# Kernel tuning notes

Hardware: AMD Instinct MI355X
Metric: run time of the kernel (lower is better)

## Reference

```python
import jax, jax.numpy as jnp
import numpy as np
import math

B, C, T = 2, 1024, 2048
H, G = 16, 32            # num_heads, groupnorm groups (channels=1024 -> 32 groups)
CH = C // H              # 64 head channels
EPS = 1e-5


def setup_inputs() -> dict:
    key = jax.random.key(0)
    ks = jax.random.split(key, 5)
    x = jax.random.normal(ks[0], (B, C, T), dtype=jnp.float32)
    # causal mask, identical across batch (matches how tortoise uses it; also makes
    # the torch mask.repeat(n_heads,1,1) tiling-order quirk a no-op)
    mask = jnp.broadcast_to(jnp.tril(jnp.ones((T, T), dtype=bool)), (B, T, T))
    qk_bias = jax.random.normal(ks[1], (1, T, T), dtype=jnp.float32) * 0.01
    gn_scale = jnp.ones((C,), dtype=jnp.float32)
    gn_bias = jnp.zeros((C,), dtype=jnp.float32)
    qkv_w = jax.random.normal(ks[2], (3 * C, C), dtype=jnp.float32) / math.sqrt(C)
    qkv_b = jnp.zeros((3 * C,), dtype=jnp.float32)
    # proj_out is zero-initialized in the module; use small random weights so the
    # attention path actually contributes (post-training regime)
    proj_w = jax.random.normal(ks[3], (C, C), dtype=jnp.float32) * 0.02
    proj_b = jnp.zeros((C,), dtype=jnp.float32)
    return {"x": x, "mask": mask, "qk_bias": qk_bias, "gn_scale": gn_scale,
            "gn_bias": gn_bias, "qkv_w": qkv_w, "qkv_b": qkv_b,
            "proj_w": proj_w, "proj_b": proj_b}


def _group_norm(x, scale, bias):
    # x: [B, C, T], normalize over (C//G, T) within each of G groups, in fp32
    xg = x.reshape(B, G, C // G, T)
    mean = xg.mean(axis=(2, 3), keepdims=True)
    var = ((xg - mean) ** 2).mean(axis=(2, 3), keepdims=True)
    xn = ((xg - mean) * jax.lax.rsqrt(var + EPS)).reshape(B, C, T)
    return xn * scale[None, :, None] + bias[None, :, None]


def reference(x, mask, qk_bias, gn_scale, gn_bias, qkv_w, qkv_b, proj_w, proj_b):
    xn = _group_norm(x, gn_scale, gn_bias)                      # [B, C, T]
    qkv = jnp.einsum('oc,bct->bot', qkv_w, xn) + qkv_b[None, :, None]  # [B, 3C, T]
    # legacy layout: width splits as (H, 3*ch)
    qkv = qkv.reshape(B * H, 3 * CH, T)
    q, k, v = qkv[:, :CH], qkv[:, CH:2 * CH], qkv[:, 2 * CH:]   # [B*H, ch, T]
    scale = 1.0 / math.sqrt(math.sqrt(CH))
    w = jnp.einsum('bct,bcs->bts', q * scale, k * scale)        # [B*H, T, T]
    w = w + qk_bias
    mask_r = jnp.tile(mask, (H, 1, 1))                          # matches torch repeat
    w = jnp.where(mask_r, w, -jnp.inf)
    w = jax.nn.softmax(w.astype(jnp.float32), axis=-1).astype(q.dtype)
    a = jnp.einsum('bts,bcs->bct', w, v).reshape(B, C, T)       # [B, C, T]
    h = jnp.einsum('oc,bct->bot', proj_w, a) + proj_b[None, :, None]
    return xn + h                                               # x_proj is Identity on normed x
```

## Files before the change

kernel.cpp:

```cpp
#include <hip/hip_runtime.h>
#include <stdint.h>

#define Tdim 2048
#define Cdim 1024
#define C3   3072

typedef __attribute__((ext_vector_type(8))) short s16x8;
typedef __attribute__((ext_vector_type(4))) unsigned short u16x4;
typedef __attribute__((ext_vector_type(2))) float f32x2;
typedef __attribute__((ext_vector_type(4))) float f32x4;
typedef __attribute__((ext_vector_type(16))) float f32x16;
typedef __attribute__((ext_vector_type(4))) int i32x4;

__device__ __forceinline__ unsigned short f2bf(float f) {
  uint32_t u = __float_as_uint(f);
  return (unsigned short)((u + 0x7FFFu + ((u >> 16) & 1u)) >> 16);
}
__device__ __forceinline__ float bf2f(unsigned short s) {
  return __uint_as_float(((uint32_t)s) << 16);
}
__device__ __forceinline__ uint32_t cvtpk(float lo, float hi) {
  uint32_t r;
  asm("v_cvt_pk_bf16_f32 %0, %1, %2" : "=v"(r) : "v"(lo), "v"(hi));
  return r;
}
__device__ __forceinline__ float exp2v(float x) {
  float r;
  asm("v_exp_f32 %0, %1" : "=v"(r) : "v"(x));
  return r;
}
typedef __attribute__((address_space(3))) unsigned char lds_uc;
typedef __attribute__((address_space(1))) const unsigned char glb_uc;
__device__ __forceinline__ void gload16(const void* g, void* l) {
  __builtin_amdgcn_global_load_lds((glb_uc*)g, (lds_uc*)l, 16, 0, 0);
}

__global__ __launch_bounds__(256) void k_prep(const float* __restrict__ x,
                                              float* __restrict__ part,
                                              const float* __restrict__ qkv_w,
                                              const float* __restrict__ proj_w,
                                              unsigned short* __restrict__ wqkv,
                                              unsigned short* __restrict__ wproj,
                                              const float* __restrict__ qk_bias,
                                              unsigned short* __restrict__ biasT) {
  __shared__ float r1[4], r2[4];
  __shared__ unsigned short L[64][65];
  int bid = blockIdx.x;
  int u = threadIdx.x;
  if (bid < 512) {
    int bg = bid >> 3, tc = bid & 7;
    const float* xp = x + ((size_t)(bg >> 5) * Cdim + (size_t)(bg & 31) * 32) * Tdim + tc * 256;
    float s1 = 0.f, s2 = 0.f;
#pragma unroll
    for (int i = 0; i < 32; ++i) {
      int e = u + i * 256;
      float v = xp[(size_t)(e >> 8) * Tdim + (e & 255)];
      s1 += v; s2 += v * v;
    }
    for (int m = 1; m < 64; m <<= 1) { s1 += __shfl_xor(s1, m); s2 += __shfl_xor(s2, m); }
    int w = u >> 6;
    if ((u & 63) == 0) { r1[w] = s1; r2[w] = s2; }
    __syncthreads();
    if (u == 0) {
      part[bid * 2]     = r1[0] + r1[1] + r1[2] + r1[3];
      part[bid * 2 + 1] = r2[0] + r2[1] + r2[2] + r2[3];
    }
  } else if (bid < 512 + 4096) {
    const int n0 = 3072 * 1024 / 4;
    int i = (bid - 512) * 256 + u;
    const float* in = qkv_w;
    unsigned short* out = wqkv;
    if (i >= n0) { i -= n0; in = proj_w; out = wproj; }
    f32x4 v = *(const f32x4*)(in + (size_t)i * 4);
    u16x4 o;
    o[0] = f2bf(v[0]); o[1] = f2bf(v[1]); o[2] = f2bf(v[2]); o[3] = f2bf(v[3]);
    *(u16x4*)(out + (size_t)i * 4) = o;
  } else {
    const float LOG2E = 1.4426950408889634f;
    int idx = bid - 4608;
    int bs0 = (idx & 31) * 64;
    int bt0 = (idx >> 5) * 64;
    int tl = u >> 2, c0 = (u & 3) * 16;
    const float* ip = qk_bias + (size_t)(bt0 + tl) * Tdim + bs0 + c0;
#pragma unroll
    for (int i = 0; i < 16; ++i) L[tl][c0 + i] = f2bf(ip[i] * LOG2E);
    __syncthreads();
    unsigned short* op = biasT + (size_t)(bs0 + tl) * Tdim + bt0 + c0;
#pragma unroll
    for (int i = 0; i < 16; i += 4) {
      u16x4 o;
      o[0] = L[c0 + i][tl]; o[1] = L[c0 + i + 1][tl];
      o[2] = L[c0 + i + 2][tl]; o[3] = L[c0 + i + 3][tl];
      *(u16x4*)(op + i) = o;
    }
  }
}

__global__ void k_gn_final(const float* __restrict__ part, float* __restrict__ stats) {
  int bg = threadIdx.x;
  float s1 = 0.f, s2 = 0.f;
  for (int j = 0; j < 8; ++j) { s1 += part[(bg * 8 + j) * 2]; s2 += part[(bg * 8 + j) * 2 + 1]; }
  const float inv = 1.f / 65536.f;
  float mean = s1 * inv;
  float var = s2 * inv - mean * mean;
  stats[bg * 2] = mean;
  stats[bg * 2 + 1] = rsqrtf(var + 1e-5f);
}

__global__ __launch_bounds__(256) void k_gn_norm(const float* __restrict__ x,
                                                 const float* __restrict__ scale,
                                                 const float* __restrict__ bias,
                                                 const float* __restrict__ stats,
                                                 unsigned short* __restrict__ xnT) {
  int ti = blockIdx.x;
  int g  = blockIdx.y;
  int b  = blockIdx.z;
  int u  = threadIdx.x;
  int bg = b * 32 + g;
  float mean = stats[bg * 2], rstd = stats[bg * 2 + 1];
  __shared__ float L[32][65];
  int c_loc = u >> 3, tc = (u & 7) * 8;
  int cg = g * 32 + c_loc;
  const float* xp = x + ((size_t)b * Cdim + cg) * Tdim + ti * 64 + tc;
  float sc = scale[cg] * rstd;
  float bi = bias[cg] - mean * sc;
#pragma unroll
  for (int i = 0; i < 8; ++i) L[c_loc][tc + i] = xp[i] * sc + bi;
  __syncthreads();
  int t_loc = u >> 2, cc = (u & 3) * 8;
  s16x8 ov;
#pragma unroll
  for (int i = 0; i < 8; ++i) ov[i] = (short)f2bf(L[cc + i][t_loc]);
  *(s16x8*)&xnT[((size_t)b * Tdim + ti * 64 + t_loc) * Cdim + g * 32 + cc] = ov;
}

__global__ __launch_bounds__(256) void k_qkv(const unsigned short* __restrict__ A,
                                             const unsigned short* __restrict__ Bw,
                                             const float* __restrict__ bias,
                                             unsigned short* __restrict__ outT) {
  const int M = 2048, N = 3072, K = 1024;
  int lin = blockIdx.x + 24 * (blockIdx.y + 16 * blockIdx.z);
  int k8 = lin & 7, j = lin >> 3;
  int bb = k8 >> 2;
  int q = k8 & 3;
  int by = (q >> 1) * 8 + j / 12;
  int bx = (q & 1) * 12 + j % 12;
  int tid = threadIdx.x;
  int lane = tid & 63, w = tid >> 6;
  int m0 = by * 128, n0 = bx * 128;
  const unsigned short* Ab = A + (size_t)bb * M * K;
  __shared__ __align__(16) short As[128 * 32];
  __shared__ __align__(16) short Bs[128 * 32];
  f32x4 acc[4][4] = {};
  int wm = (w >> 1) * 64, wn = (w & 1) * 64;
  int lr = lane & 15, lq = lane >> 4;
  int srow = w * 16 + (lane >> 2);
  int scol = (lane & 3) * 8;

  for (int k0 = 0; k0 < K; k0 += 32) {
    __syncthreads();
#pragma unroll
    for (int ch = 0; ch < 2; ++ch) {
      gload16(Ab + (size_t)(m0 + srow + ch * 64) * K + k0 + scol,
              (char*)As + w * 1024 + ch * 4096);
      gload16(Bw + (size_t)(n0 + srow + ch * 64) * K + k0 + scol,
              (char*)Bs + w * 1024 + ch * 4096);
    }
    __syncthreads();
    s16x8 af[4], bfr[4];
#pragma unroll
    for (int m = 0; m < 4; ++m) af[m] = *(const s16x8*)&As[(wm + m * 16 + lr) * 32 + lq * 8];
#pragma unroll
    for (int n = 0; n < 4; ++n) bfr[n] = *(const s16x8*)&Bs[(wn + n * 16 + lr) * 32 + lq * 8];
#pragma unroll
    for (int m = 0; m < 4; ++m)
#pragma unroll
      for (int n = 0; n < 4; ++n)
        acc[m][n] = __builtin_amdgcn_mfma_f32_16x16x32_bf16(af[m], bfr[n], acc[m][n], 0, 0, 0);
  }
#pragma unroll
  for (int n = 0; n < 4; ++n) {
    int col = n0 + wn + n * 16 + lr;
    float bv = bias[col];
#pragma unroll
    for (int m = 0; m < 4; ++m) {
      int rowb = m0 + wm + m * 16 + lq * 4;
#pragma unroll
      for (int j2 = 0; j2 < 4; ++j2)
        outT[((size_t)bb * M + rowb + j2) * N + col] = f2bf(acc[m][n][j2] + bv);
    }
  }
}

__global__ __launch_bounds__(256) void k_proj(const unsigned short* __restrict__ A,
                                              const unsigned short* __restrict__ Bw,
                                              const float* __restrict__ bias,
                                              const unsigned short* __restrict__ xnT,
                                              float* __restrict__ out) {
  const int K = 1024;
  int lin = blockIdx.x + 16 * blockIdx.y;
  int k8 = lin & 7, j = lin >> 3;
  int mt = (k8 >> 1) * 8 + (j >> 3);
  int nt = (k8 & 1) * 8 + (j & 7);
  int n0 = nt * 64, m0 = mt * 128;
  int tid = threadIdx.x;
  int lane = tid & 63, w = tid >> 6;
  __shared__ __align__(16) short As[128 * 32];
  __shared__ __align__(16) short Bs[64 * 32];
  f32x4 acc[4][2] = {};
  int wm = (w & 1) * 64, wn = (w >> 1) * 32;
  int lr = lane & 15, lq = lane >> 4;
  int srow = w * 16 + (lane >> 2);
  int scol = (lane & 3) * 8;

  for (int k0 = 0; k0 < K; k0 += 32) {
    __syncthreads();
#pragma unroll
    for (int ch = 0; ch < 2; ++ch)
      gload16(A + (size_t)(m0 + srow + ch * 64) * K + k0 + scol,
              (char*)As + w * 1024 + ch * 4096);
    gload16(Bw + (size_t)(n0 + srow) * K + k0 + scol, (char*)Bs + w * 1024);
    __syncthreads();
    s16x8 af[4], bfr[2];
#pragma unroll
    for (int m = 0; m < 4; ++m) af[m] = *(const s16x8*)&As[(wm + m * 16 + lr) * 32 + lq * 8];
#pragma unroll
    for (int n = 0; n < 2; ++n) bfr[n] = *(const s16x8*)&Bs[(wn + n * 16 + lr) * 32 + lq * 8];
#pragma unroll
    for (int m = 0; m < 4; ++m)
#pragma unroll
      for (int n = 0; n < 2; ++n)
        acc[m][n] = __builtin_amdgcn_mfma_f32_16x16x32_bf16(af[m], bfr[n], acc[m][n], 0, 0, 0);
  }
#pragma unroll
  for (int n = 0; n < 2; ++n) {
    int col = n0 + wn + n * 16 + lr;
    float bv = bias[col];
#pragma unroll
    for (int m = 0; m < 4; ++m) {
      int rowb = m0 + wm + m * 16 + lq * 4;
      int bb = rowb >> 11, t = rowb & 2047;
      f32x4 v;
#pragma unroll
      for (int j2 = 0; j2 < 4; ++j2)
        v[j2] = acc[m][n][j2] + bv + bf2f(xnT[(size_t)(rowb + j2) * Cdim + col]);
      *(f32x4*)&out[((size_t)bb * 1024 + col) * Tdim + t] = v;
    }
  }
}

__global__ __launch_bounds__(256, 2) void k_attn(const unsigned short* __restrict__ qkvT,
                                                 const unsigned short* __restrict__ biasT,
                                                 unsigned short* __restrict__ part0,
                                                 unsigned short* __restrict__ part1,
                                                 unsigned short* __restrict__ part2,
                                                 float* __restrict__ ml) {
  int lin = blockIdx.x + 32 * blockIdx.y;
  int k8 = lin & 7, j8 = lin >> 3;
  int bh = k8 * 4 + (j8 >> 5);
  int x  = j8 & 31;
  int ti, cc, nc;
  if (x < 15)      { ti = 15 - x / 3;        cc = x - (x / 3) * 3;  nc = 3; }
  else if (x < 27) { int y = x - 15; ti = 10 - (y >> 1); cc = y & 1; nc = 2; }
  else             { ti = 31 - x;            cc = 0;               nc = 1; }
  int nt_tot = 2 * ti + 2;
  int bse = nt_tot / nc, rem = nt_tot - bse * nc;
  int start = cc * bse + (cc < rem ? cc : rem);
  int cnt = bse + (cc < rem ? 1 : 0);

  int b = bh >> 4, h = bh & 15;
  int tid = threadIdx.x, lane = tid & 63, w = tid >> 6;
  int r = lane & 31, hi = lane >> 5;
  int q0 = ti * 128 + w * 32;
  int qg = q0 + r;
  const unsigned short* hb = qkvT + ((size_t)b * Tdim) * C3 + h * 192;
  const unsigned short* bT = biasT + qg;
  unsigned short* pout = (cc == 0) ? part0 : (cc == 1) ? part1 : part2;

  __shared__ __align__(16) char Ks[2][8192];
  __shared__ __align__(16) char Vt[2][8192];

  s16x8 qf[4];
#pragma unroll
  for (int kb = 0; kb < 4; ++kb) {
    s16x8 raw = *(const s16x8*)(hb + (size_t)qg * C3 + kb * 16 + hi * 8);
#pragma unroll
    for (int j = 0; j < 8; ++j)
      qf[kb][j] = (short)f2bf(bf2f((unsigned short)raw[j]) * 0.18033688011114373f);
  }

  int ksr[2], kcb[2], vsr[2], vc0[2];
#pragma unroll
  for (int p = 0; p < 2; ++p) {
    int u = tid + p * 256;
    ksr[p] = u >> 3; kcb[p] = u & 7;
    vsr[p] = u & 63; vc0[p] = (u >> 6) * 8;
  }
  s16x8 kc[2], vc[2];
  unsigned short bs[2][16];

  auto issue_kv = [&](int s0) {
#pragma unroll
    for (int p = 0; p < 2; ++p) {
      kc[p] = *(const s16x8*)(hb + (size_t)(s0 + ksr[p]) * C3 + 64 + kcb[p] * 8);
      vc[p] = *(const s16x8*)(hb + (size_t)(s0 + vsr[p]) * C3 + 128 + vc0[p]);
    }
  };
  auto issue_bias = [&](int s0) {
#pragma unroll
    for (int st = 0; st < 2; ++st)
#pragma unroll
      for (int e = 0; e < 16; ++e) {
        int s = s0 + st * 32 + (e & 3) + 8 * (e >> 2) + 4 * hi;
        bs[st][e] = bT[(size_t)s * Tdim];
      }
  };

  issue_kv(start * 64);
  issue_bias(start * 64);

  f32x16 oacc[2];
#pragma unroll
  for (int c2 = 0; c2 < 2; ++c2)
#pragma unroll
    for (int e = 0; e < 16; ++e) oacc[c2][e] = 0.f;
  float mrow = -1e30f, lrowv = 0.f;

  for (int it = 0; it < cnt; ++it) {
    int s0 = (start + it) * 64;
    int cur = it & 1;
    char* Kc = &Ks[cur][0];
    char* Vc = &Vt[cur][0];
#pragma unroll
    for (int p = 0; p < 2; ++p) {
      *(s16x8*)(Kc + ksr[p] * 128 + ((kcb[p] * 16) ^ ((ksr[p] & 7) << 4))) = kc[p];
#pragma unroll
      for (int i = 0; i < 8; ++i)
        *(short*)(Vc + (vc0[p] + i) * 128 + ((vsr[p] * 2) ^ (((vc0[p] + i) & 7) << 4))) = vc[p][i];
    }
    __syncthreads();
    if (it + 1 < cnt) issue_kv(s0 + 64);

    bool active = (s0 <= q0 + 31);
    if (active) {
      f32x16 sa[2];
#pragma unroll
      for (int st = 0; st < 2; ++st) {
#pragma unroll
        for (int e = 0; e < 16; ++e) sa[st][e] = bf2f(bs[st][e]);
        int row = st * 32 + r;
        int swz = (row & 7) << 4;
        __builtin_amdgcn_s_setprio(1);
#pragma unroll
        for (int kb = 0; kb < 4; ++kb) {
          s16x8 kf = *(const s16x8*)(Kc + row * 128 + ((kb * 32 + hi * 16) ^ swz));
          sa[st] = __builtin_amdgcn_mfma_f32_32x32x16_bf16(kf, qf[kb], sa[st], 0, 0, 0);
        }
        __builtin_amdgcn_s_setprio(0);
      }
      if (s0 + 63 > q0) {
#pragma unroll
        for (int st = 0; st < 2; ++st)
#pragma unroll
          for (int e = 0; e < 16; ++e) {
            int s = s0 + st * 32 + (e & 3) + 8 * (e >> 2) + 4 * hi;
            sa[st][e] = (s > qg) ? -1e30f : sa[st][e];
          }
      }
      if (it + 1 < cnt && s0 + 64 <= q0 + 31) issue_bias(s0 + 64);
      float t8[8];
#pragma unroll
      for (int e = 0; e < 8; ++e)
        t8[e] = fmaxf(fmaxf(sa[0][e], sa[0][e + 8]), fmaxf(sa[1][e], sa[1][e + 8]));
      float pm = fmaxf(fmaxf(fmaxf(t8[0], t8[1]), fmaxf(t8[2], t8[3])),
                       fmaxf(fmaxf(t8[4], t8[5]), fmaxf(t8[6], t8[7])));
      pm = fmaxf(pm, __shfl_xor(pm, 32));
      if (!__all(pm <= mrow + 11.5f)) {
        float mnew = fmaxf(mrow, pm);
        float al = exp2v(mrow - mnew);
        mrow = mnew;
        lrowv *= al;
#pragma unroll
        for (int c2 = 0; c2 < 2; ++c2)
#pragma unroll
          for (int e = 0; e < 16; ++e) oacc[c2][e] *= al;
      }
#pragma unroll
      for (int st = 0; st < 2; ++st)
#pragma unroll
        for (int e = 0; e < 16; ++e) sa[st][e] = exp2v(sa[st][e] - mrow);
      float s8[8];
#pragma unroll
      for (int e = 0; e < 8; ++e)
        s8[e] = (sa[0][e] + sa[0][e + 8]) + (sa[1][e] + sa[1][e + 8]);
      float rsum = ((s8[0] + s8[1]) + (s8[2] + s8[3])) + ((s8[4] + s8[5]) + (s8[6] + s8[7]));
      rsum += __shfl_xor(rsum, 32);
      lrowv += rsum;

      s16x8 pfr[4];
#pragma unroll
      for (int sblk = 0; sblk < 4; ++sblk) {
        const int st = sblk >> 1, sb = sblk & 1;
        uint32_t a0 = cvtpk(sa[st][sb * 8 + 0], sa[st][sb * 8 + 1]);
        uint32_t a1 = cvtpk(sa[st][sb * 8 + 2], sa[st][sb * 8 + 3]);
        uint32_t b0 = cvtpk(sa[st][sb * 8 + 4], sa[st][sb * 8 + 5]);
        uint32_t b1 = cvtpk(sa[st][sb * 8 + 6], sa[st][sb * 8 + 7]);
        uint32_t xa0 = (uint32_t)__shfl_xor((int)a0, 32);
        uint32_t xa1 = (uint32_t)__shfl_xor((int)a1, 32);
        uint32_t xb0 = (uint32_t)__shfl_xor((int)b0, 32);
        uint32_t xb1 = (uint32_t)__shfl_xor((int)b1, 32);
        union { i32x4 i; s16x8 s; } u;
        u.i[0] = (int)(hi ? xb0 : a0);
        u.i[1] = (int)(hi ? xb1 : a1);
        u.i[2] = (int)(hi ? b0 : xa0);
        u.i[3] = (int)(hi ? b1 : xa1);
        pfr[sblk] = u.s;
      }
      __builtin_amdgcn_s_setprio(1);
#pragma unroll
      for (int c2 = 0; c2 < 2; ++c2) {
        int row = c2 * 32 + r;
        int swz = (row & 7) << 4;
#pragma unroll
        for (int sblk = 0; sblk < 4; ++sblk) {
          s16x8 vf = *(const s16x8*)(Vc + row * 128 + ((sblk * 32 + hi * 16) ^ swz));
          oacc[c2] = __builtin_amdgcn_mfma_f32_32x32x16_bf16(vf, pfr[sblk], oacc[c2], 0, 0, 0);
        }
      }
      __builtin_amdgcn_s_setprio(0);
    }
  }

  float normf = (nc == 1) ? (1.0f / lrowv) : 1.0f;
  unsigned short* ob = pout + ((size_t)b * Tdim + qg) * Cdim + h * 64;
#pragma unroll
  for (int c2 = 0; c2 < 2; ++c2)
#pragma unroll
    for (int rg = 0; rg < 4; ++rg) {
      u16x4 o;
#pragma unroll
      for (int j = 0; j < 4; ++j) o[j] = f2bf(oacc[c2][rg * 4 + j] * normf);
      *(u16x4*)(ob + c2 * 32 + rg * 8 + 4 * hi) = o;
    }
  if (hi == 0 && nc > 1)
    *(f32x2*)(ml + ((size_t)(cc * 32 + bh) * Tdim + qg) * 2) = f32x2{mrow, lrowv};
}

__global__ __launch_bounds__(256) void k_merge(unsigned short* __restrict__ part0,
                                               const unsigned short* __restrict__ part1,
                                               const unsigned short* __restrict__ part2,
                                               const float* __restrict__ ml) {
  int idx = blockIdx.x * 256 + threadIdx.x;
  int ch8 = idx & 7;
  int q = (idx >> 3) & 2047;
  int bh = idx >> 14;
  int b = bh >> 4, h = bh & 15;
  int ti = q >> 7;
  int nc = (ti >= 11) ? 3 : (ti >= 5) ? 2 : 1;
  if (nc == 1) return;
  size_t off = ((size_t)b * Tdim + q) * Cdim + h * 64 + ch8 * 8;
  s16x8 o0 = *(const s16x8*)(part0 + off);
  f32x2 ml0 = *(const f32x2*)(ml + ((size_t)bh * Tdim + q) * 2);
  f32x2 ml1 = *(const f32x2*)(ml + ((size_t)(32 + bh) * Tdim + q) * 2);
  s16x8 o1 = *(const s16x8*)(part1 + off);
  float m = fmaxf(ml0[0], ml1[0]);
  f32x2 ml2;
  s16x8 o2;
  if (nc == 3) {
    ml2 = *(const f32x2*)(ml + ((size_t)(64 + bh) * Tdim + q) * 2);
    o2 = *(const s16x8*)(part2 + off);
    m = fmaxf(m, ml2[0]);
  }
  float e0 = exp2f(ml0[0] - m), e1 = exp2f(ml1[0] - m);
  float den = ml0[1] * e0 + ml1[1] * e1;
  float e2 = 0.f;
  if (nc == 3) { e2 = exp2f(ml2[0] - m); den += ml2[1] * e2; }
  float inv = 1.0f / den;
  float w0 = e0 * inv, w1 = e1 * inv, w2 = e2 * inv;
  s16x8 o;
#pragma unroll
  for (int i = 0; i < 8; ++i) {
    float v = bf2f((unsigned short)o0[i]) * w0 + bf2f((unsigned short)o1[i]) * w1;
    if (nc == 3) v += bf2f((unsigned short)o2[i]) * w2;
    o[i] = (short)f2bf(v);
  }
  *(s16x8*)(part0 + off) = o;
}

extern "C" void kernel_launch(void* const* d_in, const int* in_sizes, int n_in,
                              void* d_out, int out_size, void* d_ws, size_t ws_size,
                              hipStream_t stream) {
  const float* x        = (const float*)d_in[0];
  const float* qk_bias  = (const float*)d_in[2];
  const float* gn_scale = (const float*)d_in[3];
  const float* gn_bias  = (const float*)d_in[4];
  const float* qkv_w    = (const float*)d_in[5];
  const float* qkv_b    = (const float*)d_in[6];
  const float* proj_w   = (const float*)d_in[7];
  const float* proj_b   = (const float*)d_in[8];
  float* out = (float*)d_out;

  char* ws = (char*)d_ws;
  unsigned short* xnT   = (unsigned short*)(ws);
  unsigned short* qkvT  = (unsigned short*)(ws + ( 8ull << 20));
  unsigned short* aT    = (unsigned short*)(ws + (32ull << 20));
  unsigned short* part1 = (unsigned short*)(ws + (40ull << 20));
  unsigned short* wqkv  = (unsigned short*)(ws + (40ull << 20));
  unsigned short* wproj = (unsigned short*)(ws + (48ull << 20));
  float*          ml    = (float*)(ws + (50ull << 20));
  float* part  = (float*)(ws + (52ull << 20));
  float* stats = (float*)(ws + (52ull << 20) + 8192);
  unsigned short* biasT = (unsigned short*)d_out;
  unsigned short* part2 = (unsigned short*)d_out + (4ull << 20);

  k_prep<<<5632, 256, 0, stream>>>(x, part, qkv_w, proj_w, wqkv, wproj, qk_bias, biasT);
  k_gn_final<<<1, 64, 0, stream>>>(part, stats);
  k_gn_norm<<<dim3(32, 32, 2), 256, 0, stream>>>(x, gn_scale, gn_bias, stats, xnT);

  k_qkv<<<dim3(24, 16, 2), 256, 0, stream>>>(xnT, wqkv, qkv_b, qkvT);
  k_attn<<<dim3(32, 32), 256, 0, stream>>>(qkvT, biasT, aT, part1, part2, ml);
  k_merge<<<2048, 256, 0, stream>>>(aT, part1, part2, ml);
  k_proj<<<dim3(16, 32), 256, 0, stream>>>(aT, wproj, proj_b, xnT, out);
}
```

Baseline: 137.2 us.

## Rewrite QKV GEMM with 256x256 tiles, double-buffered swizzled LDS, 8 waves

The QKV projection GEMM moves from 128x128 tiles with one LDS buffer and BK=32 to 256x256 tiles with BK=64, 512 threads, and two LDS stages loaded asynchronously via global_load_lds with an XOR swizzle to avoid bank conflicts. The batch dimension is folded into M (4096 rows), so the grid becomes 192 blocks. The aim is more operand reuse per global load, and loads that overlap MFMA work instead of waiting at a barrier each iteration. The cost is 128KB of LDS per block and heavy register use for 32 accumulator tiles per wave, which may cap occupancy at one block per CU. With only 192 blocks, some of the 256 CUs also sit idle.

After: 140.4 us. 1.02x slower.

```diff
diff --git a/kernel.cpp b/kernel.cpp
--- a/kernel.cpp
+++ b/kernel.cpp
@@ -34,6 +34,8 @@
 __device__ __forceinline__ void gload16(const void* g, void* l) {
   __builtin_amdgcn_global_load_lds((glb_uc*)g, (lds_uc*)l, 16, 0, 0);
 }
+#define SBAR()  __builtin_amdgcn_s_barrier()
+#define SCHED0() __builtin_amdgcn_sched_barrier(0)
 
 __global__ __launch_bounds__(256) void k_prep(const float* __restrict__ x,
                                               float* __restrict__ part,
@@ -134,60 +136,97 @@
   *(s16x8*)&xnT[((size_t)b * Tdim + ti * 64 + t_loc) * Cdim + g * 32 + cc] = ov;
 }
 
-__global__ __launch_bounds__(256) void k_qkv(const unsigned short* __restrict__ A,
-                                             const unsigned short* __restrict__ Bw,
-                                             const float* __restrict__ bias,
-                                             unsigned short* __restrict__ outT) {
-  const int M = 2048, N = 3072, K = 1024;
-  int lin = blockIdx.x + 24 * (blockIdx.y + 16 * blockIdx.z);
+__global__ __launch_bounds__(512, 2) void k_qkv(const unsigned short* __restrict__ A,
+                                                const unsigned short* __restrict__ Bw,
+                                                const float* __restrict__ bias,
+                                                unsigned short* __restrict__ outT) {
+  const int K = 1024, N = 3072;
+  int lin = blockIdx.x;
   int k8 = lin & 7, j = lin >> 3;
-  int bb = k8 >> 2;
-  int q = k8 & 3;
-  int by = (q >> 1) * 8 + j / 12;
-  int bx = (q & 1) * 12 + j % 12;
+  int mt = (k8 >> 1) * 4 + j / 6;
+  int nt = (k8 & 1) * 6 + j % 6;
+  int m0 = mt * 256, n0 = nt * 256;
   int tid = threadIdx.x;
   int lane = tid & 63, w = tid >> 6;
-  int m0 = by * 128, n0 = bx * 128;
-  const unsigned short* Ab = A + (size_t)bb * M * K;
-  __shared__ __align__(16) short As[128 * 32];
-  __shared__ __align__(16) short Bs[128 * 32];
-  f32x4 acc[4][4] = {};
-  int wm = (w >> 1) * 64, wn = (w & 1) * 64;
+  int wm = (w >> 2) * 128, wn = (w & 3) * 64;
   int lr = lane & 15, lq = lane >> 4;
-  int srow = w * 16 + (lane >> 2);
-  int scol = (lane & 3) * 8;
-
-  for (int k0 = 0; k0 < K; k0 += 32) {
-    __syncthreads();
-#pragma unroll
-    for (int ch = 0; ch < 2; ++ch) {
-      gload16(Ab + (size_t)(m0 + srow + ch * 64) * K + k0 + scol,
-              (char*)As + w * 1024 + ch * 4096);
-      gload16(Bw + (size_t)(n0 + srow + ch * 64) * K + k0 + scol,
-              (char*)Bs + w * 1024 + ch * 4096);
-    }
-    __syncthreads();
-    s16x8 af[4], bfr[4];
-#pragma unroll
-    for (int m = 0; m < 4; ++m) af[m] = *(const s16x8*)&As[(wm + m * 16 + lr) * 32 + lq * 8];
-#pragma unroll
-    for (int n = 0; n < 4; ++n) bfr[n] = *(const s16x8*)&Bs[(wn + n * 16 + lr) * 32 + lq * 8];
-#pragma unroll
-    for (int m = 0; m < 4; ++m)
-#pragma unroll
-      for (int n = 0; n < 4; ++n)
-        acc[m][n] = __builtin_amdgcn_mfma_f32_16x16x32_bf16(af[m], bfr[n], acc[m][n], 0, 0, 0);
-  }
-#pragma unroll
-  for (int n = 0; n < 4; ++n) {
-    int col = n0 + wn + n * 16 + lr;
+
+  __shared__ __align__(16) short Asl[2][256 * 64];
+  __shared__ __align__(16) short Bsl[2][256 * 64];
+
+  int sr8 = tid >> 3;
+  int sc_base = tid & 7;
+
+  auto stage = [&](int ks, int buf) {
+#pragma unroll
+    for (int i = 0; i < 4; ++i) {
+      int row = i * 64 + sr8;
+      int scol = ((sc_base ^ (row & 7)) * 8);
+      gload16(A + (size_t)(m0 + row) * K + ks * 64 + scol,
+              (char*)&Asl[buf][0] + i * 8192 + tid * 16);
+    }
+#pragma unroll
+    for (int i = 0; i < 4; ++i) {
+      int row = i * 64 + sr8;
+      int scol = ((sc_base ^ (row & 7)) * 8);
+      gload16(Bw + (size_t)(n0 + row) * K + ks * 64 + scol,
+              (char*)&Bsl[buf][0] + i * 8192 + tid * 16);
+    }
+  };
+
+  f32x4 acc[8][4] = {};
+
+  stage(0, 0);
+  stage(1, 1);
+  asm volatile("s_waitcnt vmcnt(8)" ::: "memory");
+  SCHED0(); SBAR(); SCHED0();
+
+  for (int k = 0; k < 16; ++k) {
+    int c = k & 1;
+    const short* Al = &Asl[c][0];
+    const short* Bl = &Bsl[c][0];
+#pragma unroll
+    for (int kh = 0; kh < 2; ++kh) {
+      s16x8 af[8], bfr[4];
+#pragma unroll
+      for (int mf = 0; mf < 8; ++mf) {
+        int row = wm + mf * 16 + lr;
+        af[mf] = *(const s16x8*)((const char*)Al + row * 128 + (((kh * 4 + lq) ^ (row & 7)) * 16));
+      }
+#pragma unroll
+      for (int nf = 0; nf < 4; ++nf) {
+        int row = wn + nf * 16 + lr;
+        bfr[nf] = *(const s16x8*)((const char*)Bl + row * 128 + (((kh * 4 + lq) ^ (row & 7)) * 16));
+      }
+      __builtin_amdgcn_s_setprio(1);
+#pragma unroll
+      for (int mf = 0; mf < 8; ++mf)
+#pragma unroll
+        for (int nf = 0; nf < 4; ++nf)
+          acc[mf][nf] = __builtin_amdgcn_mfma_f32_16x16x32_bf16(af[mf], bfr[nf], acc[mf][nf], 0, 0, 0);
+      __builtin_amdgcn_s_setprio(0);
+    }
+    asm volatile("s_waitcnt lgkmcnt(0)" ::: "memory");
+    SCHED0(); SBAR(); SCHED0();
+    if (k + 2 < 16) {
+      stage(k + 2, c);
+      asm volatile("s_waitcnt vmcnt(8)" ::: "memory");
+    } else {
+      asm volatile("s_waitcnt vmcnt(0)" ::: "memory");
+    }
+    SCHED0(); SBAR(); SCHED0();
+  }
+
+#pragma unroll
+  for (int nf = 0; nf < 4; ++nf) {
+    int col = n0 + wn + nf * 16 + lr;
     float bv = bias[col];
 #pragma unroll
-    for (int m = 0; m < 4; ++m) {
-      int rowb = m0 + wm + m * 16 + lq * 4;
+    for (int mf = 0; mf < 8; ++mf) {
+      int rowf = m0 + wm + mf * 16 + lq * 4;
 #pragma unroll
       for (int j2 = 0; j2 < 4; ++j2)
-        outT[((size_t)bb * M + rowb + j2) * N + col] = f2bf(acc[m][n][j2] + bv);
+        outT[(size_t)(rowf + j2) * N + col] = f2bf(acc[mf][nf][j2] + bv);
     }
   }
 }
@@ -517,7 +556,7 @@
   k_gn_final<<<1, 64, 0, stream>>>(part, stats);
   k_gn_norm<<<dim3(32, 32, 2), 256, 0, stream>>>(x, gn_scale, gn_bias, stats, xnT);
 
-  k_qkv<<<dim3(24, 16, 2), 256, 0, stream>>>(xnT, wqkv, qkv_b, qkvT);
+  k_qkv<<<192, 512, 0, stream>>>(xnT, wqkv, qkv_b, qkvT);
   k_attn<<<dim3(32, 32), 256, 0, stream>>>(qkvT, biasT, aT, part1, part2, ml);
   k_merge<<<2048, 256, 0, stream>>>(aT, part1, part2, ml);
   k_proj<<<dim3(16, 32), 256, 0, stream>>>(aT, wproj, proj_b, xnT, out);
```
